# Kernel optimization log

Measured on AMD Instinct MI355X. Metric: run time of the kernel, lower is better.

The kernel has to match this reference:

```python
import jax, jax.numpy as jnp
import numpy as np

OUT_CH = 64
K = 7

def setup_inputs() -> dict:
    key = jax.random.key(0)
    k1, k2 = jax.random.split(key)
    data = jax.random.normal(k1, (32, 1, 224, 224), dtype=jnp.float32)
    # torch Conv2d default init: uniform(-b, b), b = 1/sqrt(in_ch*k*k)
    bound = 1.0 / np.sqrt(1 * K * K)
    weight = jax.random.uniform(k2, (OUT_CH, 1, K, K), dtype=jnp.float32,
                                minval=-bound, maxval=bound)
    return {"data": data, "weight": weight}

def reference(data, weight):
    # Valid (padding=0) stride-1 conv, NCHW x OIHW -> NCHW
    return jax.lax.conv_general_dilated(
        data, weight,
        window_strides=(1, 1),
        padding="VALID",
        dimension_numbers=("NCHW", "OIHW", "NCHW"),
    )
```

## Files before the change

kernel.cpp:

```cpp
#include <hip/hip_runtime.h>
#include <hip/hip_bf16.h>

#define IN_H  224
#define IN_W  224
#define OUT_H 218
#define OUT_W 218
#define NCH   64
#define PLANE (OUT_H * OUT_W)
#define RSH   464
#define CP1   232
#define NROW  4
#define NYB   55
#define NMT   4
#define OCH   876
#define NBLK  (32 * NMT * NYB)

typedef short bf16x8 __attribute__((ext_vector_type(8)));
typedef float f32x4  __attribute__((ext_vector_type(4)));

__device__ inline unsigned int f2bf(float f) {
    unsigned int u = __builtin_bit_cast(unsigned int, f);
    return (u + 0x7fffu + ((u >> 16) & 1u)) >> 16;
}

__device__ inline unsigned int pk2(float lo, float hi) {
    __hip_bfloat162 h2 = __float22bfloat162_rn(make_float2(lo, hi));
    unsigned int u;
    __builtin_memcpy(&u, &h2, sizeof(u));
    return u;
}

__global__ __launch_bounds__(512) void repack_w(const float* __restrict__ wgt,
                                                unsigned int* __restrict__ wa) {
    const int t    = threadIdx.x;
    const int lane = t & 63;
    const int fc   = t >> 6;
    const int mt   = fc >> 1, kt = fc & 1;
    const int ch   = 16 * mt + (lane & 15);
    const int dy   = 4 * kt + (lane >> 4);
    unsigned int w[4];
#pragma unroll
    for (int j = 0; j < 4; ++j) {
        float lo = (dy < 7 && 2 * j     < 7) ? wgt[ch * 49 + dy * 7 + 2 * j]     : 0.f;
        float hi = (dy < 7 && 2 * j + 1 < 7) ? wgt[ch * 49 + dy * 7 + 2 * j + 1] : 0.f;
        w[j] = f2bf(lo) | (f2bf(hi) << 16);
    }
    reinterpret_cast<uint4*>(wa)[fc * 64 + lane] = make_uint4(w[0], w[1], w[2], w[3]);
}

__global__ __launch_bounds__(512) void conv7x7_row(
    const float* __restrict__ in,
    const unsigned int* __restrict__ wa,
    float* __restrict__ out)
{
    __shared__ unsigned short tbf[10 * RSH];
    __shared__ float obuf[16 * OCH];

    const int tid  = threadIdx.x;
    const int lane = tid & 63;
    const int wid  = tid >> 6;
    const int g    = lane >> 4;
    const int c    = lane & 15;

    const int bid  = blockIdx.x;
    const int rank = (bid & 7) * (NBLK / 8) + (bid >> 3);
    const int n    = rank / (NMT * NYB);
    const int rem  = rank - n * (NMT * NYB);
    const int mt   = rem / NYB;
    const int yb   = rem - mt * NYB;
    const int y0   = yb * NROW;

    union AB { uint4 u; bf16x8 v; };
    AB af[2];
    const uint4* wa4 = reinterpret_cast<const uint4*>(wa);
#pragma unroll
    for (int kt = 0; kt < 2; ++kt) af[kt].u = wa4[(mt * 2 + kt) * 64 + lane];

    const float* inb = in + (size_t)n * (IN_H * IN_W);
    for (int idx = tid; idx < 10 * 112; idx += 512) {
        int r = idx / 112, c2 = idx - r * 112;
        int iny = min(y0 + r, IN_H - 1);
        const float* rp = inb + iny * IN_W + 2 * c2;
        float2 v = *reinterpret_cast<const float2*>(rp);
        float nx = (c2 < 111) ? rp[2] : 0.f;
        *reinterpret_cast<unsigned int*>(&tbf[r * RSH + 2 * c2]) = pk2(v.x, v.y);
        *reinterpret_cast<unsigned int*>(&tbf[r * RSH + CP1 + 2 * c2]) = pk2(v.y, nx);
    }
    for (int idx = tid; idx < 10 * 8; idx += 512) {
        int r = idx >> 3, j = idx & 7;
        *reinterpret_cast<unsigned int*>(&tbf[r * RSH + (j >> 2) * CP1 + 224 + 2 * (j & 3)]) = 0u;
    }
    __syncthreads();

    const int sh = c & 1;
    for (int k = wid; k < 4 * 14; k += 8) {
        const int r  = k / 14;
        const int x0 = 16 * (k - 14 * r);
        const int e0 = x0 + c - sh;

        AB bf[2];
#pragma unroll
        for (int kt = 0; kt < 2; ++kt) {
            const int row = min(r + 4 * kt + g, 9);
            const unsigned int* p = reinterpret_cast<const unsigned int*>(
                &tbf[row * RSH + sh * CP1 + e0]);
            union { unsigned int u[4]; uint4 q; } bb;
            bb.u[0] = p[0]; bb.u[1] = p[1]; bb.u[2] = p[2]; bb.u[3] = p[3];
            bf[kt].u = bb.q;
        }

        f32x4 acc = {0.f, 0.f, 0.f, 0.f};
        acc = __builtin_amdgcn_mfma_f32_16x16x32_bf16(af[0].v, bf[0].v, acc, 0, 0, 0);
        acc = __builtin_amdgcn_mfma_f32_16x16x32_bf16(af[1].v, bf[1].v, acc, 0, 0, 0);

        if (x0 + c < OUT_W) {
#pragma unroll
            for (int rr = 0; rr < 4; ++rr)
                obuf[(4 * g + rr) * OCH + r * OUT_W + x0 + c] = acc[rr];
        }
    }
    __syncthreads();

    const int vrows = min(NROW, OUT_H - y0);
    const int nf4   = (vrows * OUT_W) >> 2;
    const size_t base = ((size_t)(n * NCH + 16 * mt)) * PLANE + (size_t)y0 * OUT_W;
#pragma unroll
    for (int i = 0; i < 2; ++i) {
        const int p = 2 * wid + i;
        const float* src = &obuf[p * OCH];
        float* dst = out + base + (size_t)p * PLANE;
#pragma unroll
        for (int j = 0; j < 4; ++j) {
            int idx = 64 * j + lane;
            if (idx < nf4)
                *reinterpret_cast<float4*>(dst + 4 * idx) =
                    *reinterpret_cast<const float4*>(src + 4 * idx);
        }
    }
}

extern "C" void kernel_launch(void* const* d_in, const int* in_sizes, int n_in,
                              void* d_out, int out_size, void* d_ws, size_t ws_size,
                              hipStream_t stream) {
    const float* in  = (const float*)d_in[0];
    const float* wgt = (const float*)d_in[1];
    float* out = (float*)d_out;
    unsigned int* wa = (unsigned int*)d_ws;

    repack_w<<<1, 512, 0, stream>>>(wgt, wa);
    conv7x7_row<<<NBLK, 512, 0, stream>>>(in, wa, out);
}
```

Before: 86.72 us.

## Split conv into two row halves so global stores overlap the second half's MFMA

The tile-staging loop now loads float4 per thread and writes 8-byte packed bf16 pairs, and the separate zero-padding loop is folded into it. The compute phase is split into two halves of two output rows each. A custom barrier waits only on LDS counters (lgkmcnt) before s_barrier, so the global stores of the first half can be issued while the second half computes, instead of waiting for all compute. The risks are the extra barrier, and hand-written waitcnt semantics that depend on global stores not being tracked by lgkmcnt.

```diff
diff --git a/kernel.cpp b/kernel.cpp
--- a/kernel.cpp
+++ b/kernel.cpp
@@ -28,6 +28,13 @@
     unsigned int u;
     __builtin_memcpy(&u, &h2, sizeof(u));
     return u;
+}
+
+__device__ inline void bar_lgkm() {
+    asm volatile("s_waitcnt lgkmcnt(0)" ::: "memory");
+    __builtin_amdgcn_sched_barrier(0);
+    __builtin_amdgcn_s_barrier();
+    __builtin_amdgcn_sched_barrier(0);
 }
 
 __global__ __launch_bounds__(512) void repack_w(const float* __restrict__ wgt,
@@ -77,66 +84,77 @@
     for (int kt = 0; kt < 2; ++kt) af[kt].u = wa4[(mt * 2 + kt) * 64 + lane];
 
     const float* inb = in + (size_t)n * (IN_H * IN_W);
-    for (int idx = tid; idx < 10 * 112; idx += 512) {
-        int r = idx / 112, c2 = idx - r * 112;
+    for (int idx = tid; idx < 10 * 58; idx += 512) {
+        int r = idx / 58, c4 = idx - r * 58;
         int iny = min(y0 + r, IN_H - 1);
-        const float* rp = inb + iny * IN_W + 2 * c2;
-        float2 v = *reinterpret_cast<const float2*>(rp);
-        float nx = (c2 < 111) ? rp[2] : 0.f;
-        *reinterpret_cast<unsigned int*>(&tbf[r * RSH + 2 * c2]) = pk2(v.x, v.y);
-        *reinterpret_cast<unsigned int*>(&tbf[r * RSH + CP1 + 2 * c2]) = pk2(v.y, nx);
-    }
-    for (int idx = tid; idx < 10 * 8; idx += 512) {
-        int r = idx >> 3, j = idx & 7;
-        *reinterpret_cast<unsigned int*>(&tbf[r * RSH + (j >> 2) * CP1 + 224 + 2 * (j & 3)]) = 0u;
+        const float* rp = inb + iny * IN_W;
+        float4 v = (c4 < 56) ? *reinterpret_cast<const float4*>(rp + 4 * c4)
+                             : make_float4(0.f, 0.f, 0.f, 0.f);
+        float nx = (c4 < 55) ? rp[4 * c4 + 4] : 0.f;
+        uint2 w0 = make_uint2(pk2(v.x, v.y), pk2(v.z, v.w));
+        uint2 w1 = make_uint2(pk2(v.y, v.z), pk2(v.w, nx));
+        *reinterpret_cast<uint2*>(&tbf[r * RSH + 4 * c4])       = w0;
+        *reinterpret_cast<uint2*>(&tbf[r * RSH + CP1 + 4 * c4]) = w1;
     }
     __syncthreads();
 
     const int sh = c & 1;
-    for (int k = wid; k < 4 * 14; k += 8) {
-        const int r  = k / 14;
-        const int x0 = 16 * (k - 14 * r);
-        const int e0 = x0 + c - sh;
 
-        AB bf[2];
-#pragma unroll
-        for (int kt = 0; kt < 2; ++kt) {
-            const int row = min(r + 4 * kt + g, 9);
-            const unsigned int* p = reinterpret_cast<const unsigned int*>(
-                &tbf[row * RSH + sh * CP1 + e0]);
-            union { unsigned int u[4]; uint4 q; } bb;
-            bb.u[0] = p[0]; bb.u[1] = p[1]; bb.u[2] = p[2]; bb.u[3] = p[3];
-            bf[kt].u = bb.q;
-        }
+#define CONV_ITER(kk)                                                          \
+    {                                                                          \
+        const int r  = (kk) / 14;                                              \
+        const int x0 = 16 * ((kk) - 14 * r);                                   \
+        const int e0 = x0 + c - sh;                                            \
+        AB bf[2];                                                              \
+        _Pragma("unroll")                                                      \
+        for (int kt = 0; kt < 2; ++kt) {                                       \
+            const int row = min(r + 4 * kt + g, 9);                            \
+            const unsigned int* p = reinterpret_cast<const unsigned int*>(     \
+                &tbf[row * RSH + sh * CP1 + e0]);                              \
+            union { unsigned int u[4]; uint4 q; } bb;                          \
+            bb.u[0] = p[0]; bb.u[1] = p[1]; bb.u[2] = p[2]; bb.u[3] = p[3];    \
+            bf[kt].u = bb.q;                                                   \
+        }                                                                      \
+        f32x4 acc = {0.f, 0.f, 0.f, 0.f};                                      \
+        acc = __builtin_amdgcn_mfma_f32_16x16x32_bf16(af[0].v, bf[0].v, acc, 0, 0, 0); \
+        acc = __builtin_amdgcn_mfma_f32_16x16x32_bf16(af[1].v, bf[1].v, acc, 0, 0, 0); \
+        if (x0 + c < OUT_W) {                                                  \
+            _Pragma("unroll")                                                  \
+            for (int rr = 0; rr < 4; ++rr)                                     \
+                obuf[(4 * g + rr) * OCH + r * OUT_W + x0 + c] = acc[rr];       \
+        }                                                                      \
+    }
 
-        f32x4 acc = {0.f, 0.f, 0.f, 0.f};
-        acc = __builtin_amdgcn_mfma_f32_16x16x32_bf16(af[0].v, bf[0].v, acc, 0, 0, 0);
-        acc = __builtin_amdgcn_mfma_f32_16x16x32_bf16(af[1].v, bf[1].v, acc, 0, 0, 0);
+#define STORE_HALF(srcoff, n4)                                                 \
+    {                                                                          \
+        const size_t base = ((size_t)(n * NCH + 16 * mt)) * PLANE              \
+                          + (size_t)y0 * OUT_W + (srcoff);                     \
+        _Pragma("unroll")                                                      \
+        for (int i = 0; i < 2; ++i) {                                          \
+            const int p = 2 * wid + i;                                         \
+            const float* src = &obuf[p * OCH + (srcoff)];                      \
+            float* dst = out + base + (size_t)p * PLANE;                       \
+            _Pragma("unroll")                                                  \
+            for (int j = 0; j < 2; ++j) {                                      \
+                int idx = 64 * j + lane;                                       \
+                if (idx < (n4))                                                \
+                    *reinterpret_cast<float4*>(dst + 4 * idx) =                \
+                        *reinterpret_cast<const float4*>(src + 4 * idx);       \
+            }                                                                  \
+        }                                                                      \
+    }
 
-        if (x0 + c < OUT_W) {
-#pragma unroll
-            for (int rr = 0; rr < 4; ++rr)
-                obuf[(4 * g + rr) * OCH + r * OUT_W + x0 + c] = acc[rr];
-        }
-    }
-    __syncthreads();
+    for (int k = wid; k < 28; k += 8) CONV_ITER(k)
+    bar_lgkm();
 
-    const int vrows = min(NROW, OUT_H - y0);
-    const int nf4   = (vrows * OUT_W) >> 2;
-    const size_t base = ((size_t)(n * NCH + 16 * mt)) * PLANE + (size_t)y0 * OUT_W;
-#pragma unroll
-    for (int i = 0; i < 2; ++i) {
-        const int p = 2 * wid + i;
-        const float* src = &obuf[p * OCH];
-        float* dst = out + base + (size_t)p * PLANE;
-#pragma unroll
-        for (int j = 0; j < 4; ++j) {
-            int idx = 64 * j + lane;
-            if (idx < nf4)
-                *reinterpret_cast<float4*>(dst + 4 * idx) =
-                    *reinterpret_cast<const float4*>(src + 4 * idx);
-        }
-    }
+    STORE_HALF(0, 109)
+    for (int k = 28 + wid; k < 56; k += 8) CONV_ITER(k)
+    bar_lgkm();
+
+    if (y0 + 2 < OUT_H) STORE_HALF(436, 109)
+
+#undef CONV_ITER
+#undef STORE_HALF
 }
 
 extern "C" void kernel_launch(void* const* d_in, const int* in_sizes, int n_in,
```

After: 88.45 us. About the same (+2.0%).
